# Kernel tuning notes

Measured on AMD Instinct MI355X. Metric: run time of the kernel, lower is better.

Reference implementation:

```python
import jax, jax.numpy as jnp
import numpy as np

B, N, D, K, H = 32768, 17, 2, 3, 64


def _mlp_params(key, n, d_in, d_hid, d_out):
    k1, k2, k3, k4 = jax.random.split(key, 4)
    W1 = jax.random.normal(k1, (n, d_in, d_hid), jnp.float32) / np.sqrt(d_in)
    b1 = jnp.zeros((n, d_hid), jnp.float32)
    W2 = jax.random.normal(k2, (n, d_hid, d_out), jnp.float32) / np.sqrt(d_hid)
    b2 = jnp.zeros((n, d_out), jnp.float32)
    return W1, b1, W2, b2


def setup_inputs() -> dict:
    key = jax.random.key(0)
    kp, kk, kw, kb = jax.random.split(key, 4)
    pred_pts = jax.random.normal(kp, (B, N, D), jnp.float32)
    kW1, kb1, kW2, kb2 = _mlp_params(kk, N, D, H, K)            # k_nets
    wW1, wb1, wW2, wb2 = _mlp_params(kw, N, D, H, K)            # weight_nets
    bW1, bb1, bW2, bb2 = _mlp_params(kb, N, D, 2 * H, K * 2 * D)  # basis_nets
    return dict(pred_pts=pred_pts,
                kW1=kW1, kb1=kb1, kW2=kW2, kb2=kb2,
                wW1=wW1, wb1=wb1, wW2=wW2, wb2=wb2,
                bW1=bW1, bb1=bb1, bW2=bW2, bb2=bb2)


def _per_joint_mlp(x, W1, b1, W2, b2):
    # x: [B,N,D]; W1: [N,D,Hd]; W2: [N,Hd,O]
    h = jax.nn.relu(jnp.einsum('bnd,ndh->bnh', x, W1) + b1[None])
    return jnp.einsum('bnh,nho->bno', h, W2) + b2[None]


def reference(pred_pts, kW1, kb1, kW2, kb2, wW1, wb1, wW2, wb2, bW1, bb1, bW2, bb2):
    Bc, Nc, Dc = pred_pts.shape
    Kc = kW2.shape[-1]

    # k-selection head (eval mode: argmax, +1)
    k_logits = _per_joint_mlp(pred_pts, kW1, kb1, kW2, kb2)      # [B,N,K]
    k_js = jnp.argmax(k_logits, axis=-1) + 1                     # [B,N] int

    # mixture weights
    w = jax.nn.softmax(_per_joint_mlp(pred_pts, wW1, wb1, wW2, wb2), axis=-1)  # [B,N,K]

    # basis parameters: mu, sigma = exp(log_sigma)
    params = _per_joint_mlp(pred_pts, bW1, bb1, bW2, bb2).reshape(Bc, Nc, Kc, 2 * Dc)
    mu = params[..., :Dc]                                         # [B,N,K,D]
    sigma = jnp.exp(params[..., Dc:])                             # [B,N,K,D]

    # top-k selection by descending weight (indices are constants w.r.t. grad)
    idx = jnp.argsort(-w, axis=-1)                                # [B,N,K]
    mu_top = jnp.take_along_axis(mu, idx[..., None], axis=2)      # [B,N,K,D]
    sigma_top = jnp.take_along_axis(sigma, idx[..., None], axis=2)
    mask = jnp.arange(Kc)[None, None, :] < k_js[..., None]        # [B,N,K] bool

    # pack float outputs: weights + selected (mu, sigma) -> [B,N,K,1+2D]
    out = jnp.concatenate([w[..., None], mu_top, sigma_top], axis=-1)
    return out, k_js, mask
```

## Files before the change

kernel.cpp:

```cpp
#include <hip/hip_runtime.h>
#include <cmath>

#define NBATCH 32768
#define NJOINT 17
#define OUT0_ELEMS (NBATCH * NJOINT * 15)
#define KJS_OFF    OUT0_ELEMS
#define MASK_OFF   (KJS_OFF + NBATCH * NJOINT)

#define WN_STRIDE 774
#define WS_DOUBLES (NJOINT * WN_STRIDE)

__device__ __forceinline__ float sel3f(int i, float a, float b, float c) {
    return (i == 0) ? a : ((i == 1) ? b : c);
}

__global__ void cvt_weights_f64(
    const float* __restrict__ kW1, const float* __restrict__ kb1,
    const float* __restrict__ kW2, const float* __restrict__ kb2,
    const float* __restrict__ wW1, const float* __restrict__ wb1,
    const float* __restrict__ wW2, const float* __restrict__ wb2,
    double* __restrict__ dws)
{
    const int n = blockIdx.x;
    double* o = dws + (size_t)n * WN_STRIDE;
    for (int i = threadIdx.x; i < WN_STRIDE; i += blockDim.x) {
        int j = i;
        const float* W1 = kW1; const float* b1 = kb1;
        const float* W2 = kW2; const float* b2 = kb2;
        if (j >= 387) { j -= 387; W1 = wW1; b1 = wb1; W2 = wW2; b2 = wb2; }
        float v;
        if (j < 128)      v = W1[n * 128 + j];
        else if (j < 192) v = b1[n * 64 + (j - 128)];
        else if (j < 384) v = W2[n * 192 + (j - 192)];
        else              v = b2[n * 3 + (j - 384)];
        o[i] = (double)v;
    }
}

template<bool USE_WS>
__device__ __forceinline__ void compute_point(
    int n, float x0f, float x1f,
    const float* __restrict__ kW1, const float* __restrict__ kb1,
    const float* __restrict__ kW2, const float* __restrict__ kb2,
    const float* __restrict__ wW1, const float* __restrict__ wb1,
    const float* __restrict__ wW2, const float* __restrict__ wb2,
    const float* __restrict__ bW1, const float* __restrict__ bb1,
    const float* __restrict__ bW2, const float* __restrict__ bb2,
    const double* __restrict__ dws,
    float r[15], int& kj_out)
{
    const double x0 = (double)x0f, x1 = (double)x1f;
    double kl0, kl1, kl2, wl0, wl1, wl2;

    if constexpr (USE_WS) {
        const double* Wn = dws + (size_t)n * WN_STRIDE;
        {
            const double* W1a = Wn;
            const double* W1b = Wn + 64;
            const double* b1  = Wn + 128;
            const double* W2  = Wn + 192;
            kl0 = Wn[384]; kl1 = Wn[385]; kl2 = Wn[386];
            #pragma unroll 4
            for (int h = 0; h < 64; ++h) {
                double hv = fmax(fma(x1, W1b[h], fma(x0, W1a[h], b1[h])), 0.0);
                kl0 = fma(hv, W2[h * 3 + 0], kl0);
                kl1 = fma(hv, W2[h * 3 + 1], kl1);
                kl2 = fma(hv, W2[h * 3 + 2], kl2);
            }
        }
        {
            const double* W1a = Wn + 387;
            const double* W1b = Wn + 451;
            const double* b1  = Wn + 515;
            const double* W2  = Wn + 579;
            wl0 = Wn[771]; wl1 = Wn[772]; wl2 = Wn[773];
            #pragma unroll 4
            for (int h = 0; h < 64; ++h) {
                double hv = fmax(fma(x1, W1b[h], fma(x0, W1a[h], b1[h])), 0.0);
                wl0 = fma(hv, W2[h * 3 + 0], wl0);
                wl1 = fma(hv, W2[h * 3 + 1], wl1);
                wl2 = fma(hv, W2[h * 3 + 2], wl2);
            }
        }
    } else {
        {
            const float* W1a = kW1 + n * 128;
            const float* W1b = W1a + 64;
            const float* b1  = kb1 + n * 64;
            const float* W2  = kW2 + n * 192;
            kl0 = (double)kb2[n * 3 + 0];
            kl1 = (double)kb2[n * 3 + 1];
            kl2 = (double)kb2[n * 3 + 2];
            #pragma unroll 4
            for (int h = 0; h < 64; ++h) {
                double hv = fma(x1, (double)W1b[h], fma(x0, (double)W1a[h], (double)b1[h]));
                hv = fmax(hv, 0.0);
                kl0 = fma(hv, (double)W2[h * 3 + 0], kl0);
                kl1 = fma(hv, (double)W2[h * 3 + 1], kl1);
                kl2 = fma(hv, (double)W2[h * 3 + 2], kl2);
            }
        }
        {
            const float* W1a = wW1 + n * 128;
            const float* W1b = W1a + 64;
            const float* b1  = wb1 + n * 64;
            const float* W2  = wW2 + n * 192;
            wl0 = (double)wb2[n * 3 + 0];
            wl1 = (double)wb2[n * 3 + 1];
            wl2 = (double)wb2[n * 3 + 2];
            #pragma unroll 4
            for (int h = 0; h < 64; ++h) {
                double hv = fma(x1, (double)W1b[h], fma(x0, (double)W1a[h], (double)b1[h]));
                hv = fmax(hv, 0.0);
                wl0 = fma(hv, (double)W2[h * 3 + 0], wl0);
                wl1 = fma(hv, (double)W2[h * 3 + 1], wl1);
                wl2 = fma(hv, (double)W2[h * 3 + 2], wl2);
            }
        }
    }

    int kj = 0;
    {
        double m = kl0;
        if (kl1 > m) { m = kl1; kj = 1; }
        if (kl2 > m) { kj = 2; }
    }
    kj_out = kj;

    int i0 = 0;
    {
        double m = wl0;
        if (wl1 > m) { m = wl1; i0 = 1; }
        if (wl2 > m) { i0 = 2; }
    }
    const int ia = (i0 == 0) ? 1 : 0;
    const int ib = (i0 == 2) ? 1 : 2;
    const double wa = ia ? wl1 : wl0;
    const double wb = (ib == 1) ? wl1 : wl2;
    const int i1 = (wb > wa) ? ib : ia;
    const int i2 = (wb > wa) ? ia : ib;

    const double mw = fmax(fmax(wl0, wl1), wl2);
    const float e0 = __expf((float)(wl0 - mw));
    const float e1 = __expf((float)(wl1 - mw));
    const float e2 = __expf((float)(wl2 - mw));
    const float inv = 1.0f / (e0 + e1 + e2);
    const float p0 = e0 * inv, p1 = e1 * inv, p2 = e2 * inv;

    float acc[12];
    {
        const float* W1a = bW1 + n * 256;
        const float* W1b = W1a + 128;
        const float* b1  = bb1 + n * 128;
        const float* W2  = bW2 + n * 1536;
        const float* b2  = bb2 + n * 12;
        #pragma unroll
        for (int j = 0; j < 12; ++j) acc[j] = b2[j];
        #pragma unroll 4
        for (int h = 0; h < 128; ++h) {
            float hv = fmaxf(fmaf(x1f, W1b[h], fmaf(x0f, W1a[h], b1[h])), 0.0f);
            #pragma unroll
            for (int j = 0; j < 12; ++j)
                acc[j] = fmaf(hv, W2[h * 12 + j], acc[j]);
        }
    }

    r[0]  = p0; r[5] = p1; r[10] = p2;
    r[1]  = sel3f(i0, acc[0], acc[4], acc[8]);
    r[2]  = sel3f(i0, acc[1], acc[5], acc[9]);
    r[3]  = __expf(sel3f(i0, acc[2], acc[6], acc[10]));
    r[4]  = __expf(sel3f(i0, acc[3], acc[7], acc[11]));
    r[6]  = sel3f(i1, acc[0], acc[4], acc[8]);
    r[7]  = sel3f(i1, acc[1], acc[5], acc[9]);
    r[8]  = __expf(sel3f(i1, acc[2], acc[6], acc[10]));
    r[9]  = __expf(sel3f(i1, acc[3], acc[7], acc[11]));
    r[11] = sel3f(i2, acc[0], acc[4], acc[8]);
    r[12] = sel3f(i2, acc[1], acc[5], acc[9]);
    r[13] = __expf(sel3f(i2, acc[2], acc[6], acc[10]));
    r[14] = __expf(sel3f(i2, acc[3], acc[7], acc[11]));
}

template<bool USE_WS>
__global__ __launch_bounds__(256) void mdn_fused(
    const float* __restrict__ pred_pts,
    const float* __restrict__ kW1, const float* __restrict__ kb1,
    const float* __restrict__ kW2, const float* __restrict__ kb2,
    const float* __restrict__ wW1, const float* __restrict__ wb1,
    const float* __restrict__ wW2, const float* __restrict__ wb2,
    const float* __restrict__ bW1, const float* __restrict__ bb1,
    const float* __restrict__ bW2, const float* __restrict__ bb2,
    float* __restrict__ out,
    const double* __restrict__ dws)
{
    const int l    = threadIdx.x;
    const int w    = l >> 6;
    const int lane = l & 63;
    const int bx   = blockIdx.x;
    const int by   = blockIdx.y;
    const int n0   = by * 4;

    int n = n0 + w;
    if (n >= NJOINT) return;
    n = __builtin_amdgcn_readfirstlane(n);

    const int b = bx * 64 + lane;
    const int p = b * NJOINT + n;

    const float2 xv = *reinterpret_cast<const float2*>(pred_pts + 2 * p);

    float r[15];
    int kj;
    compute_point<USE_WS>(n, xv.x, xv.y,
                          kW1, kb1, kW2, kb2, wW1, wb1, wW2, wb2,
                          bW1, bb1, bW2, bb2, dws, r, kj);

    if (by == 4) {
        float* o = out + (size_t)p * 15;
        #pragma unroll
        for (int i = 0; i < 15; ++i) o[i] = r[i];
        out[KJS_OFF + p] = (float)(kj + 1);
        float* mk = out + MASK_OFF + (size_t)p * 3;
        mk[0] = 1.0f;
        mk[1] = (kj >= 1) ? 1.0f : 0.0f;
        mk[2] = (kj >= 2) ? 1.0f : 0.0f;
        return;
    }

    __shared__ float s_out[256 * 17];
    {
        float* so = s_out + (w * 64 + lane) * 17;
        #pragma unroll
        for (int j = 0; j < 15; ++j) so[j] = r[j];
        so[15] = (float)(kj + 1);
    }
    __syncthreads();

    if (l < 240) {
        const int c_off = l / 60;
        const int jj    = l - c_off * 60;
        const int nl    = jj / 15;
        const int j     = jj - nl * 15;
        const int lbase = nl * 1088 + c_off * 17 + j;
        size_t g = (size_t)((bx * 64 + c_off) * NJOINT + n0) * 15 + jj;
        #pragma unroll
        for (int rr = 0; rr < 16; ++rr) {
            out[g] = s_out[lbase + 68 * rr];
            g += 1020;
        }
    }

    {
        const int bl  = l >> 2;
        const int nlr = l & 3;
        const float kjf = s_out[(nlr * 64 + bl) * 17 + 15];
        const int pg = (bx * 64 + bl) * NJOINT + n0 + nlr;
        out[KJS_OFF + pg] = kjf;
        float* mk = out + MASK_OFF + (size_t)pg * 3;
        mk[0] = 1.0f;
        mk[1] = (kjf >= 1.5f) ? 1.0f : 0.0f;
        mk[2] = (kjf >= 2.5f) ? 1.0f : 0.0f;
    }
}

extern "C" void kernel_launch(void* const* d_in, const int* in_sizes, int n_in,
                              void* d_out, int out_size, void* d_ws, size_t ws_size,
                              hipStream_t stream) {
    (void)in_sizes; (void)n_in; (void)out_size;
    const bool use_ws = (d_ws != nullptr) && (ws_size >= (size_t)WS_DOUBLES * sizeof(double));
    dim3 grid(NBATCH / 64, 5);
    if (use_ws) {
        cvt_weights_f64<<<NJOINT, 256, 0, stream>>>(
            (const float*)d_in[1], (const float*)d_in[2],
            (const float*)d_in[3], (const float*)d_in[4],
            (const float*)d_in[5], (const float*)d_in[6],
            (const float*)d_in[7], (const float*)d_in[8],
            (double*)d_ws);
        mdn_fused<true><<<grid, 256, 0, stream>>>(
            (const float*)d_in[0],
            (const float*)d_in[1], (const float*)d_in[2],
            (const float*)d_in[3], (const float*)d_in[4],
            (const float*)d_in[5], (const float*)d_in[6],
            (const float*)d_in[7], (const float*)d_in[8],
            (const float*)d_in[9], (const float*)d_in[10],
            (const float*)d_in[11], (const float*)d_in[12],
            (float*)d_out, (const double*)d_ws);
    } else {
        mdn_fused<false><<<grid, 256, 0, stream>>>(
            (const float*)d_in[0],
            (const float*)d_in[1], (const float*)d_in[2],
            (const float*)d_in[3], (const float*)d_in[4],
            (const float*)d_in[5], (const float*)d_in[6],
            (const float*)d_in[7], (const float*)d_in[8],
            (const float*)d_in[9], (const float*)d_in[10],
            (const float*)d_in[11], (const float*)d_in[12],
            (float*)d_out, nullptr);
    }
}
```

Before: 145.6 us.

## Process two batch points per thread to reuse weight loads across points

Each thread now evaluates two batch elements (lane and lane+64) per joint. Every weight load (scalar/uniform since joint is wave-uniform) is shared across both points' FMAs, halving weight-fetch overhead per point. The tile grows to 128 batches per block, shared staging is doubled, and launch_bounds adds a min-blocks hint of 4. The cost is higher register pressure from two sets of fp64 and fp32 accumulators, and half as many blocks in the grid.

After: 150.2 us. 1.03x slower.

```diff
diff --git a/kernel.cpp b/kernel.cpp
--- a/kernel.cpp
+++ b/kernel.cpp
@@ -9,6 +9,7 @@
 
 #define WN_STRIDE 774
 #define WS_DOUBLES (NJOINT * WN_STRIDE)
+#define TILE_B   128
 
 __device__ __forceinline__ float sel3f(int i, float a, float b, float c) {
     return (i == 0) ? a : ((i == 1) ? b : c);
@@ -37,97 +38,70 @@
     }
 }
 
-template<bool USE_WS>
-__device__ __forceinline__ void compute_point(
-    int n, float x0f, float x1f,
-    const float* __restrict__ kW1, const float* __restrict__ kb1,
-    const float* __restrict__ kW2, const float* __restrict__ kb2,
-    const float* __restrict__ wW1, const float* __restrict__ wb1,
-    const float* __restrict__ wW2, const float* __restrict__ wb2,
-    const float* __restrict__ bW1, const float* __restrict__ bb1,
-    const float* __restrict__ bW2, const float* __restrict__ bb2,
-    const double* __restrict__ dws,
-    float r[15], int& kj_out)
-{
-    const double x0 = (double)x0f, x1 = (double)x1f;
-    double kl0, kl1, kl2, wl0, wl1, wl2;
-
-    if constexpr (USE_WS) {
-        const double* Wn = dws + (size_t)n * WN_STRIDE;
-        {
-            const double* W1a = Wn;
-            const double* W1b = Wn + 64;
-            const double* b1  = Wn + 128;
-            const double* W2  = Wn + 192;
-            kl0 = Wn[384]; kl1 = Wn[385]; kl2 = Wn[386];
-            #pragma unroll 4
-            for (int h = 0; h < 64; ++h) {
-                double hv = fmax(fma(x1, W1b[h], fma(x0, W1a[h], b1[h])), 0.0);
-                kl0 = fma(hv, W2[h * 3 + 0], kl0);
-                kl1 = fma(hv, W2[h * 3 + 1], kl1);
-                kl2 = fma(hv, W2[h * 3 + 2], kl2);
-            }
-        }
-        {
-            const double* W1a = Wn + 387;
-            const double* W1b = Wn + 451;
-            const double* b1  = Wn + 515;
-            const double* W2  = Wn + 579;
-            wl0 = Wn[771]; wl1 = Wn[772]; wl2 = Wn[773];
-            #pragma unroll 4
-            for (int h = 0; h < 64; ++h) {
-                double hv = fmax(fma(x1, W1b[h], fma(x0, W1a[h], b1[h])), 0.0);
-                wl0 = fma(hv, W2[h * 3 + 0], wl0);
-                wl1 = fma(hv, W2[h * 3 + 1], wl1);
-                wl2 = fma(hv, W2[h * 3 + 2], wl2);
-            }
-        }
-    } else {
-        {
-            const float* W1a = kW1 + n * 128;
-            const float* W1b = W1a + 64;
-            const float* b1  = kb1 + n * 64;
-            const float* W2  = kW2 + n * 192;
-            kl0 = (double)kb2[n * 3 + 0];
-            kl1 = (double)kb2[n * 3 + 1];
-            kl2 = (double)kb2[n * 3 + 2];
-            #pragma unroll 4
-            for (int h = 0; h < 64; ++h) {
-                double hv = fma(x1, (double)W1b[h], fma(x0, (double)W1a[h], (double)b1[h]));
-                hv = fmax(hv, 0.0);
-                kl0 = fma(hv, (double)W2[h * 3 + 0], kl0);
-                kl1 = fma(hv, (double)W2[h * 3 + 1], kl1);
-                kl2 = fma(hv, (double)W2[h * 3 + 2], kl2);
-            }
-        }
-        {
-            const float* W1a = wW1 + n * 128;
-            const float* W1b = W1a + 64;
-            const float* b1  = wb1 + n * 64;
-            const float* W2  = wW2 + n * 192;
-            wl0 = (double)wb2[n * 3 + 0];
-            wl1 = (double)wb2[n * 3 + 1];
-            wl2 = (double)wb2[n * 3 + 2];
-            #pragma unroll 4
-            for (int h = 0; h < 64; ++h) {
-                double hv = fma(x1, (double)W1b[h], fma(x0, (double)W1a[h], (double)b1[h]));
-                hv = fmax(hv, 0.0);
-                wl0 = fma(hv, (double)W2[h * 3 + 0], wl0);
-                wl1 = fma(hv, (double)W2[h * 3 + 1], wl1);
-                wl2 = fma(hv, (double)W2[h * 3 + 2], wl2);
-            }
-        }
-    }
-
-    int kj = 0;
+__device__ __forceinline__ void mlp64_ws_2(
+    const double* __restrict__ gws,
+    double xA0, double xA1, double xB0, double xB1,
+    double& lA0, double& lA1, double& lA2,
+    double& lB0, double& lB1, double& lB2)
+{
+    const double* W1a = gws;
+    const double* W1b = gws + 64;
+    const double* b1  = gws + 128;
+    const double* W2  = gws + 192;
+    lA0 = gws[384]; lA1 = gws[385]; lA2 = gws[386];
+    lB0 = gws[384]; lB1 = gws[385]; lB2 = gws[386];
+    #pragma unroll 4
+    for (int h = 0; h < 64; ++h) {
+        const double wa = W1a[h], wb = W1b[h], bb = b1[h];
+        const double w0 = W2[h * 3 + 0], w1 = W2[h * 3 + 1], w2 = W2[h * 3 + 2];
+        double hvA = fmax(fma(xA1, wb, fma(xA0, wa, bb)), 0.0);
+        double hvB = fmax(fma(xB1, wb, fma(xB0, wa, bb)), 0.0);
+        lA0 = fma(hvA, w0, lA0); lB0 = fma(hvB, w0, lB0);
+        lA1 = fma(hvA, w1, lA1); lB1 = fma(hvB, w1, lB1);
+        lA2 = fma(hvA, w2, lA2); lB2 = fma(hvB, w2, lB2);
+    }
+}
+
+__device__ __forceinline__ void mlp64_cvt_2(
+    const float* __restrict__ W1, const float* __restrict__ b1f,
+    const float* __restrict__ W2f, const float* __restrict__ b2f, int n,
+    double xA0, double xA1, double xB0, double xB1,
+    double& lA0, double& lA1, double& lA2,
+    double& lB0, double& lB1, double& lB2)
+{
+    const float* W1a = W1 + n * 128;
+    const float* W1b = W1a + 64;
+    const float* b1  = b1f + n * 64;
+    const float* W2  = W2f + n * 192;
+    lA0 = (double)b2f[n * 3 + 0]; lB0 = lA0;
+    lA1 = (double)b2f[n * 3 + 1]; lB1 = lA1;
+    lA2 = (double)b2f[n * 3 + 2]; lB2 = lA2;
+    #pragma unroll 4
+    for (int h = 0; h < 64; ++h) {
+        const double wa = (double)W1a[h], wb = (double)W1b[h], bb = (double)b1[h];
+        const double w0 = (double)W2[h * 3 + 0], w1 = (double)W2[h * 3 + 1],
+                     w2 = (double)W2[h * 3 + 2];
+        double hvA = fmax(fma(xA1, wb, fma(xA0, wa, bb)), 0.0);
+        double hvB = fmax(fma(xB1, wb, fma(xB0, wa, bb)), 0.0);
+        lA0 = fma(hvA, w0, lA0); lB0 = fma(hvB, w0, lB0);
+        lA1 = fma(hvA, w1, lA1); lB1 = fma(hvB, w1, lB1);
+        lA2 = fma(hvA, w2, lA2); lB2 = fma(hvB, w2, lB2);
+    }
+}
+
+__device__ __forceinline__ void decide(
+    double kl0, double kl1, double kl2,
+    double wl0, double wl1, double wl2,
+    int& kj, int& i0, int& i1, int& i2,
+    float& p0, float& p1, float& p2)
+{
+    kj = 0;
     {
         double m = kl0;
         if (kl1 > m) { m = kl1; kj = 1; }
         if (kl2 > m) { kj = 2; }
     }
-    kj_out = kj;
-
-    int i0 = 0;
+    i0 = 0;
     {
         double m = wl0;
         if (wl1 > m) { m = wl1; i0 = 1; }
@@ -137,34 +111,21 @@
     const int ib = (i0 == 2) ? 1 : 2;
     const double wa = ia ? wl1 : wl0;
     const double wb = (ib == 1) ? wl1 : wl2;
-    const int i1 = (wb > wa) ? ib : ia;
-    const int i2 = (wb > wa) ? ia : ib;
+    i1 = (wb > wa) ? ib : ia;
+    i2 = (wb > wa) ? ia : ib;
 
     const double mw = fmax(fmax(wl0, wl1), wl2);
     const float e0 = __expf((float)(wl0 - mw));
     const float e1 = __expf((float)(wl1 - mw));
     const float e2 = __expf((float)(wl2 - mw));
     const float inv = 1.0f / (e0 + e1 + e2);
-    const float p0 = e0 * inv, p1 = e1 * inv, p2 = e2 * inv;
-
-    float acc[12];
-    {
-        const float* W1a = bW1 + n * 256;
-        const float* W1b = W1a + 128;
-        const float* b1  = bb1 + n * 128;
-        const float* W2  = bW2 + n * 1536;
-        const float* b2  = bb2 + n * 12;
-        #pragma unroll
-        for (int j = 0; j < 12; ++j) acc[j] = b2[j];
-        #pragma unroll 4
-        for (int h = 0; h < 128; ++h) {
-            float hv = fmaxf(fmaf(x1f, W1b[h], fmaf(x0f, W1a[h], b1[h])), 0.0f);
-            #pragma unroll
-            for (int j = 0; j < 12; ++j)
-                acc[j] = fmaf(hv, W2[h * 12 + j], acc[j]);
-        }
-    }
-
+    p0 = e0 * inv; p1 = e1 * inv; p2 = e2 * inv;
+}
+
+__device__ __forceinline__ void epilogue(
+    const float acc[12], int i0, int i1, int i2,
+    float p0, float p1, float p2, float r[15])
+{
     r[0]  = p0; r[5] = p1; r[10] = p2;
     r[1]  = sel3f(i0, acc[0], acc[4], acc[8]);
     r[2]  = sel3f(i0, acc[1], acc[5], acc[9]);
@@ -181,7 +142,67 @@
 }
 
 template<bool USE_WS>
-__global__ __launch_bounds__(256) void mdn_fused(
+__device__ __forceinline__ void compute2(
+    int n, float xA0f, float xA1f, float xB0f, float xB1f,
+    const float* __restrict__ kW1, const float* __restrict__ kb1,
+    const float* __restrict__ kW2, const float* __restrict__ kb2,
+    const float* __restrict__ wW1, const float* __restrict__ wb1,
+    const float* __restrict__ wW2, const float* __restrict__ wb2,
+    const float* __restrict__ bW1, const float* __restrict__ bb1,
+    const float* __restrict__ bW2, const float* __restrict__ bb2,
+    const double* __restrict__ dws,
+    float rA[15], float rB[15], int& kjA, int& kjB)
+{
+    const double xA0 = (double)xA0f, xA1 = (double)xA1f;
+    const double xB0 = (double)xB0f, xB1 = (double)xB1f;
+
+    double klA0, klA1, klA2, klB0, klB1, klB2;
+    double wlA0, wlA1, wlA2, wlB0, wlB1, wlB2;
+    if constexpr (USE_WS) {
+        const double* Wn = dws + (size_t)n * WN_STRIDE;
+        mlp64_ws_2(Wn,       xA0, xA1, xB0, xB1, klA0, klA1, klA2, klB0, klB1, klB2);
+        mlp64_ws_2(Wn + 387, xA0, xA1, xB0, xB1, wlA0, wlA1, wlA2, wlB0, wlB1, wlB2);
+    } else {
+        mlp64_cvt_2(kW1, kb1, kW2, kb2, n, xA0, xA1, xB0, xB1,
+                    klA0, klA1, klA2, klB0, klB1, klB2);
+        mlp64_cvt_2(wW1, wb1, wW2, wb2, n, xA0, xA1, xB0, xB1,
+                    wlA0, wlA1, wlA2, wlB0, wlB1, wlB2);
+    }
+
+    int i0A, i1A, i2A, i0B, i1B, i2B;
+    float p0A, p1A, p2A, p0B, p1B, p2B;
+    decide(klA0, klA1, klA2, wlA0, wlA1, wlA2, kjA, i0A, i1A, i2A, p0A, p1A, p2A);
+    decide(klB0, klB1, klB2, wlB0, wlB1, wlB2, kjB, i0B, i1B, i2B, p0B, p1B, p2B);
+
+    float accA[12], accB[12];
+    {
+        const float* W1a = bW1 + n * 256;
+        const float* W1b = W1a + 128;
+        const float* b1  = bb1 + n * 128;
+        const float* W2  = bW2 + n * 1536;
+        const float* b2  = bb2 + n * 12;
+        #pragma unroll
+        for (int j = 0; j < 12; ++j) { accA[j] = b2[j]; accB[j] = b2[j]; }
+        #pragma unroll 4
+        for (int h = 0; h < 128; ++h) {
+            const float wa = W1a[h], wb = W1b[h], bb = b1[h];
+            float hvA = fmaxf(fmaf(xA1f, wb, fmaf(xA0f, wa, bb)), 0.0f);
+            float hvB = fmaxf(fmaf(xB1f, wb, fmaf(xB0f, wa, bb)), 0.0f);
+            #pragma unroll
+            for (int j = 0; j < 12; ++j) {
+                const float wv = W2[h * 12 + j];
+                accA[j] = fmaf(hvA, wv, accA[j]);
+                accB[j] = fmaf(hvB, wv, accB[j]);
+            }
+        }
+    }
+
+    epilogue(accA, i0A, i1A, i2A, p0A, p1A, p2A, rA);
+    epilogue(accB, i0B, i1B, i2B, p0B, p1B, p2B, rB);
+}
+
+template<bool USE_WS>
+__global__ __launch_bounds__(256, 4) void mdn_fused(
     const float* __restrict__ pred_pts,
     const float* __restrict__ kW1, const float* __restrict__ kb1,
     const float* __restrict__ kW2, const float* __restrict__ kb2,
@@ -203,35 +224,42 @@
     if (n >= NJOINT) return;
     n = __builtin_amdgcn_readfirstlane(n);
 
-    const int b = bx * 64 + lane;
-    const int p = b * NJOINT + n;
-
-    const float2 xv = *reinterpret_cast<const float2*>(pred_pts + 2 * p);
-
-    float r[15];
-    int kj;
-    compute_point<USE_WS>(n, xv.x, xv.y,
-                          kW1, kb1, kW2, kb2, wW1, wb1, wW2, wb2,
-                          bW1, bb1, bW2, bb2, dws, r, kj);
+    const int bA = bx * TILE_B + lane;
+    const int bB = bA + 64;
+    const int pA = bA * NJOINT + n;
+    const int pB = bB * NJOINT + n;
+
+    const float2 xA = *reinterpret_cast<const float2*>(pred_pts + 2 * pA);
+    const float2 xB = *reinterpret_cast<const float2*>(pred_pts + 2 * pB);
+
+    float rA[15], rB[15];
+    int kjA, kjB;
+    compute2<USE_WS>(n, xA.x, xA.y, xB.x, xB.y,
+                     kW1, kb1, kW2, kb2, wW1, wb1, wW2, wb2,
+                     bW1, bb1, bW2, bb2, dws, rA, rB, kjA, kjB);
 
     if (by == 4) {
-        float* o = out + (size_t)p * 15;
+        float* oA = out + (size_t)pA * 15;
+        float* oB = out + (size_t)pB * 15;
         #pragma unroll
-        for (int i = 0; i < 15; ++i) o[i] = r[i];
-        out[KJS_OFF + p] = (float)(kj + 1);
-        float* mk = out + MASK_OFF + (size_t)p * 3;
-        mk[0] = 1.0f;
-        mk[1] = (kj >= 1) ? 1.0f : 0.0f;
-        mk[2] = (kj >= 2) ? 1.0f : 0.0f;
+        for (int i = 0; i < 15; ++i) { oA[i] = rA[i]; oB[i] = rB[i]; }
+        out[KJS_OFF + pA] = (float)(kjA + 1);
+        out[KJS_OFF + pB] = (float)(kjB + 1);
+        float* mkA = out + MASK_OFF + (size_t)pA * 3;
+        mkA[0] = 1.0f; mkA[1] = (kjA >= 1) ? 1.0f : 0.0f; mkA[2] = (kjA >= 2) ? 1.0f : 0.0f;
+        float* mkB = out + MASK_OFF + (size_t)pB * 3;
+        mkB[0] = 1.0f; mkB[1] = (kjB >= 1) ? 1.0f : 0.0f; mkB[2] = (kjB >= 2) ? 1.0f : 0.0f;
         return;
     }
 
-    __shared__ float s_out[256 * 17];
+    __shared__ float s_out[512 * 17];
     {
-        float* so = s_out + (w * 64 + lane) * 17;
+        float* soA = s_out + (w * TILE_B + lane) * 17;
+        float* soB = soA + 64 * 17;
         #pragma unroll
-        for (int j = 0; j < 15; ++j) so[j] = r[j];
-        so[15] = (float)(kj + 1);
+        for (int j = 0; j < 15; ++j) { soA[j] = rA[j]; soB[j] = rB[j]; }
+        soA[15] = (float)(kjA + 1);
+        soB[15] = (float)(kjB + 1);
     }
     __syncthreads();
 
@@ -240,20 +268,22 @@
         const int jj    = l - c_off * 60;
         const int nl    = jj / 15;
         const int j     = jj - nl * 15;
-        const int lbase = nl * 1088 + c_off * 17 + j;
-        size_t g = (size_t)((bx * 64 + c_off) * NJOINT + n0) * 15 + jj;
+        const int lbase = (nl * TILE_B + c_off) * 17 + j;
+        size_t g = (size_t)((bx * TILE_B + c_off) * NJOINT + n0) * 15 + jj;
         #pragma unroll
-        for (int rr = 0; rr < 16; ++rr) {
+        for (int rr = 0; rr < 32; ++rr) {
             out[g] = s_out[lbase + 68 * rr];
             g += 1020;
         }
     }
 
-    {
-        const int bl  = l >> 2;
-        const int nlr = l & 3;
-        const float kjf = s_out[(nlr * 64 + bl) * 17 + 15];
-        const int pg = (bx * 64 + bl) * NJOINT + n0 + nlr;
+    #pragma unroll
+    for (int it = 0; it < 2; ++it) {
+        const int q   = it * 256 + l;
+        const int bl  = q >> 2;
+        const int nlr = q & 3;
+        const float kjf = s_out[(nlr * TILE_B + bl) * 17 + 15];
+        const int pg = (bx * TILE_B + bl) * NJOINT + n0 + nlr;
         out[KJS_OFF + pg] = kjf;
         float* mk = out + MASK_OFF + (size_t)pg * 3;
         mk[0] = 1.0f;
@@ -267,7 +297,7 @@
                               hipStream_t stream) {
     (void)in_sizes; (void)n_in; (void)out_size;
     const bool use_ws = (d_ws != nullptr) && (ws_size >= (size_t)WS_DOUBLES * sizeof(double));
-    dim3 grid(NBATCH / 64, 5);
+    dim3 grid(NBATCH / TILE_B, 5);
     if (use_ws) {
         cvt_weights_f64<<<NJOINT, 256, 0, stream>>>(
             (const float*)d_in[1], (const float*)d_in[2],
```
